# Kernel tuning notes

Measured on AMD Instinct MI355X. Metric: run time of the kernel, lower is better.

Reference implementation:

```python
import jax, jax.numpy as jnp
import numpy as np

CH = 512
RED = 16

def setup_inputs() -> dict:
    key = jax.random.key(0)
    ks = jax.random.split(key, 8)
    cq = CH // RED
    s = 0.02
    return {
        "x": jax.random.normal(ks[0], (4, CH, 64, 64), dtype=jnp.float32),
        "wq": jax.random.normal(ks[1], (cq, CH), dtype=jnp.float32) * s,
        "bq": jnp.zeros((cq,), dtype=jnp.float32),
        "wk": jax.random.normal(ks[2], (cq, CH), dtype=jnp.float32) * s,
        "bk": jnp.zeros((cq,), dtype=jnp.float32),
        "wv": jax.random.normal(ks[3], (CH, CH), dtype=jnp.float32) * s,
        "bv": jnp.zeros((CH,), dtype=jnp.float32),
        "gamma_pa": jnp.zeros((1,), dtype=jnp.float32),
        "gamma_ca": jnp.zeros((1,), dtype=jnp.float32),
    }

def _position_attention(x, wq, bq, wk, bk, wv, bv, gamma):
    B, C, H, W = x.shape
    xf = x.reshape(B, C, H * W)                     # [B, C, N]
    # 1x1 convs = per-pixel linear maps over channels
    q = jnp.einsum('oc,bcn->bon', wq, xf) + bq[None, :, None]   # [B, Cq, N]
    k = jnp.einsum('oc,bcn->bon', wk, xf) + bk[None, :, None]   # [B, Cq, N]
    v = jnp.einsum('oc,bcn->bon', wv, xf) + bv[None, :, None]   # [B, C,  N]
    # attention over key positions, no sqrt(d) scaling (faithful to DANet)
    energy = jnp.einsum('bcn,bcm->bnm', q, k)       # [B, N, N]
    attn = jax.nn.softmax(energy, axis=-1)
    out = jnp.einsum('bcm,bnm->bcn', v, attn)       # value @ attn^T
    out = out.reshape(B, C, H, W)
    return gamma * out + x

def _channel_attention(x, gamma):
    B, C, H, W = x.shape
    xf = x.reshape(B, C, H * W)                     # [B, C, N]
    energy = jnp.einsum('bcn,bdn->bcd', xf, xf)     # [B, C, C]
    energy_new = jnp.max(energy, axis=-1, keepdims=True) - energy
    attn = jax.nn.softmax(energy_new, axis=-1)
    out = jnp.einsum('bcd,bdn->bcn', attn, xf).reshape(B, C, H, W)
    return gamma * out + x

def reference(x, wq, bq, wk, bk, wv, bv, gamma_pa, gamma_ca):
    pa = _position_attention(x, wq, bq, wk, bk, wv, bv, gamma_pa)
    ca = _channel_attention(x, gamma_ca)
    return pa + ca
```

## Files before the change

### kernel.cpp

```cpp
#include <hip/hip_runtime.h>

#define CH   512
#define NPIX 4096
#define CQ   32
#define MR   640
#define NB   4

typedef unsigned short u16;
typedef __bf16 bf16x8 __attribute__((ext_vector_type(8)));
typedef float  f32x4  __attribute__((ext_vector_type(4)));
typedef unsigned int uint4v __attribute__((ext_vector_type(4)));
typedef unsigned int uint2v __attribute__((ext_vector_type(2)));

__device__ __forceinline__ u16 f2bf(float f) {
  union { float f; unsigned int u; } v; v.f = f;
  unsigned int r = v.u + 0x7FFFu + ((v.u >> 16) & 1u);
  return (u16)(r >> 16);
}

__device__ __forceinline__ void gload_lds16(const u16* g, u16* l) {
  __builtin_amdgcn_global_load_lds(
      (const __attribute__((address_space(1))) unsigned int*)g,
      (__attribute__((address_space(3))) unsigned int*)l, 16, 0, 0);
}

__device__ __forceinline__ int xcd_swz(int flat, int nwg) {
  if (nwg & 7) return flat;
  return (flat & 7) * (nwg >> 3) + (flat >> 3);
}

__global__ void k_prep_w(const float* __restrict__ wq, const float* __restrict__ bq,
                         const float* __restrict__ wk, const float* __restrict__ bk,
                         const float* __restrict__ wv, const float* __restrict__ bv,
                         u16* __restrict__ Wb, float* __restrict__ biasS) {
  int idx = blockIdx.x * 256 + threadIdx.x;
  if (idx < MR * CH) {
    int r = idx >> 9, c = idx & 511;
    float v = 0.f;
    if (r < 512)      v = wv[r * CH + c];
    else if (r < 544) v = wq[(r - 512) * CH + c];
    else if (r < 576) v = wk[(r - 544) * CH + c];
    Wb[idx] = f2bf(v);
  }
  if (idx < MR) {
    float v = 0.f;
    if (idx < 512)      v = bv[idx];
    else if (idx < 544) v = bq[idx - 512];
    else if (idx < 576) v = bk[idx - 544];
    biasS[idx] = v;
  }
}

__global__ __launch_bounds__(256) void k_convert(const float* __restrict__ x,
                                                 u16* __restrict__ Xb,
                                                 u16* __restrict__ Xt) {
  __shared__ float tile[64][65];
  const int b = blockIdx.z, ct = blockIdx.y, nt = blockIdx.x;
  const int t = threadIdx.x, tn = t & 63, tg = t >> 6;
  const size_t xbase = ((size_t)b * CH + ct * 64) * NPIX + nt * 64;
#pragma unroll
  for (int i = 0; i < 16; ++i) {
    int cl = tg * 16 + i;
    float v = x[xbase + (size_t)cl * NPIX + tn];
    Xb[xbase + (size_t)cl * NPIX + tn] = f2bf(v);
    tile[cl][tn] = v;
  }
  __syncthreads();
  const size_t tbase = ((size_t)b * NPIX + nt * 64) * CH + ct * 64;
#pragma unroll
  for (int i = 0; i < 16; ++i) {
    int nl = tg * 16 + i;
    Xt[tbase + (size_t)nl * CH + tn] = f2bf(tile[tn][nl]);
  }
}

enum { EP_QKV = 0, EP_PART = 1 };

template <int EP>
__global__ __launch_bounds__(256) void gemm_nt(
    const u16* __restrict__ Aall, const u16* __restrict__ Ball,
    long sA, long sB, int K, int ld, int zBase,
    void* pa0, void* pa1, void* pa2, const float* pg) {
  __shared__ u16 Alds[128 * 32];
  __shared__ u16 Blds[128 * 32];
  const int nbx = gridDim.x, nby = gridDim.y;
  const int nwg = nbx * nby * gridDim.z;
  int flat = blockIdx.x + nbx * (blockIdx.y + nby * blockIdx.z);
  flat = xcd_swz(flat, nwg);
  const int bx = flat % nbx, by = (flat / nbx) % nby, bz = flat / (nbx * nby);

  const int t = threadIdx.x, l = t & 63, w = t >> 6;
  const int wr = w >> 1, wc = w & 1;
  size_t aoff, boff;
  if constexpr (EP == EP_PART) {
    aoff = (size_t)(bz >> 2) * sA + (size_t)(bz & 3) * 1024;
    boff = (size_t)(bz >> 2) * sB + (size_t)(bz & 3) * 1024;
  } else {
    aoff = (size_t)bz * sA;
    boff = (size_t)bz * sB;
  }
  const u16* A = Aall + aoff;
  const u16* B = Ball + boff;
  const int rowBase = bx * 128, colBase = by * 128;

  f32x4 acc[4][4];
#pragma unroll
  for (int i = 0; i < 4; ++i)
#pragma unroll
    for (int j = 0; j < 4; ++j) acc[i][j] = f32x4{0.f, 0.f, 0.f, 0.f};

  const int rs0 = l >> 2, cs0 = (l & 3) * 8;

  for (int k0 = 0; k0 < K; k0 += 32) {
    __syncthreads();
#pragma unroll
    for (int i = 0; i < 2; ++i) {
      int chunk = w * 2 + i;
      int r = chunk * 16 + rs0;
      gload_lds16(A + (size_t)(rowBase + r) * ld + k0 + cs0, Alds + chunk * 512);
      gload_lds16(B + (size_t)(colBase + r) * ld + k0 + cs0, Blds + chunk * 512);
    }
    __syncthreads();
    bf16x8 af[4], bfr[4];
#pragma unroll
    for (int i = 0; i < 4; ++i) {
      af[i]  = *(const bf16x8*)(Alds + (wr * 64 + i * 16 + (l & 15)) * 32 + (l >> 4) * 8);
      bfr[i] = *(const bf16x8*)(Blds + (wc * 64 + i * 16 + (l & 15)) * 32 + (l >> 4) * 8);
    }
#pragma unroll
    for (int i = 0; i < 4; ++i)
#pragma unroll
      for (int j = 0; j < 4; ++j)
        acc[i][j] = __builtin_amdgcn_mfma_f32_16x16x32_bf16(af[i], bfr[j], acc[i][j], 0, 0, 0);
  }

  const int b = zBase + bz;
  if constexpr (EP == EP_QKV) {
    u16* Vb = (u16*)pa0; u16* Qt = (u16*)pa1; u16* Kt = (u16*)pa2;
#pragma unroll
    for (int i = 0; i < 4; ++i)
#pragma unroll
      for (int r = 0; r < 4; ++r) {
        int row = rowBase + wr * 64 + i * 16 + (l >> 4) * 4 + r;
        if (row >= 576) continue;
        float bias = pg[row];
#pragma unroll
        for (int j = 0; j < 4; ++j) {
          int col = colBase + wc * 64 + j * 16 + (l & 15);
          u16 h = f2bf(acc[i][j][r] + bias);
          if (row < 512)      Vb[((size_t)b * CH + row) * NPIX + col] = h;
          else if (row < 544) Qt[((size_t)b * NPIX + col) * CQ + (row - 512)] = h;
          else                Kt[((size_t)b * NPIX + col) * CQ + (row - 544)] = h;
        }
      }
  } else {
    float* C = (float*)pa0;
#pragma unroll
    for (int i = 0; i < 4; ++i)
#pragma unroll
      for (int j = 0; j < 4; ++j)
#pragma unroll
        for (int r = 0; r < 4; ++r) {
          int row = rowBase + wr * 64 + i * 16 + (l >> 4) * 4 + r;
          int col = colBase + wc * 64 + j * 16 + (l & 15);
          C[((size_t)bz * CH + row) * CH + col] = acc[i][j][r];
        }
  }
}

__global__ __launch_bounds__(256, 2) void k_pa_fused(
    const u16* __restrict__ Qt, const u16* __restrict__ Kt,
    const u16* __restrict__ Vb, const u16* __restrict__ Aca,
    const u16* __restrict__ Xt, const float* __restrict__ x,
    float* __restrict__ out, const float* __restrict__ gpa) {
  __shared__ u16 Plds[64 * 64];
  __shared__ u16 Vlds[2][4][64 * 64];
  int flat = xcd_swz(blockIdx.x, gridDim.x);
  const int chalf = flat & 1, nt = (flat >> 1) & 63, b = flat >> 7;
  const int n0 = nt * 64;
  const int l = threadIdx.x & 63, w = threadIdx.x >> 6;
  const int lo = l & 15, hi = l >> 4;
  const int c0w = chalf * 256 + w * 64;

  const u16* Qtb = Qt + (size_t)b * NPIX * CQ;
  const u16* Ktb = Kt + (size_t)b * NPIX * CQ;
  const u16* Vbb = Vb + (size_t)b * CH * NPIX;
  const f32x4 zero = {0.f, 0.f, 0.f, 0.f};

  bf16x8 bq[4];
#pragma unroll
  for (int nf = 0; nf < 4; ++nf)
    bq[nf] = *(const bf16x8*)(Qtb + (size_t)(n0 + nf * 16 + lo) * CQ + hi * 8);

  f32x4 acc[4][4];
#pragma unroll
  for (int i = 0; i < 4; ++i)
#pragma unroll
    for (int j = 0; j < 4; ++j) acc[i][j] = zero;
  float rs[4] = {0.f, 0.f, 0.f, 0.f};

  const int vcolsw = (((l & 7) ^ (l >> 3)) << 3);
  const u16* vsrc0 = Vbb + (size_t)(c0w + (l >> 3)) * NPIX + vcolsw;

#define LDK(m) (*(const bf16x8*)(Ktb + (size_t)((m) + w * 16 + lo) * CQ + hi * 8))
#define STAGE_V(mm, X)                                                         \
  {                                                                            \
    u16* vb_ = &Vlds[X][w][0];                                                 \
    const u16* g_ = vsrc0 + (mm);                                              \
    _Pragma("unroll")                                                          \
    for (int s_ = 0; s_ < 8; ++s_)                                             \
      gload_lds16(g_ + (size_t)s_ * 8 * NPIX, vb_ + s_ * 512);                 \
  }

  bf16x8 kc = LDK(0), kn;
  STAGE_V(0, 0);
  const int pslot = w * 2 + (hi >> 1);

  for (int ti = 0; ti < 64; ++ti) {
    const int X = ti & 1;
    const int mnext = ((ti + 1) & 63) * 64;
    f32x4 s[4];
#pragma unroll
    for (int nf = 0; nf < 4; ++nf)
      s[nf] = __builtin_amdgcn_mfma_f32_16x16x32_bf16(kc, bq[nf], zero, 0, 0, 0);
    kn = LDK(mnext);
    unsigned int uu[4][2];
#pragma unroll
    for (int nf = 0; nf < 4; ++nf) {
      float p0 = __expf(s[nf][0]), p1 = __expf(s[nf][1]);
      float p2 = __expf(s[nf][2]), p3 = __expf(s[nf][3]);
      rs[nf] += (p0 + p1) + (p2 + p3);
      asm("v_cvt_pk_bf16_f32 %0, %1, %2" : "=v"(uu[nf][0]) : "v"(p0), "v"(p1));
      asm("v_cvt_pk_bf16_f32 %0, %1, %2" : "=v"(uu[nf][1]) : "v"(p2), "v"(p3));
    }
    __builtin_amdgcn_s_barrier();
    __builtin_amdgcn_sched_barrier(0);
#pragma unroll
    for (int nf = 0; nf < 4; ++nf) {
      int n_ = nf * 16 + lo;
      char* dst_ = (char*)Plds + n_ * 128 + ((pslot ^ (n_ & 7)) << 4) + (hi & 1) * 8;
      *(uint2v*)dst_ = uint2v{uu[nf][0], uu[nf][1]};
    }
    asm volatile("s_waitcnt lgkmcnt(0)" ::: "memory");
    __builtin_amdgcn_sched_barrier(0);
    __builtin_amdgcn_s_barrier();
    __builtin_amdgcn_sched_barrier(0);
    STAGE_V(mnext, X ^ 1);
    asm volatile("s_waitcnt vmcnt(9)" ::: "memory");
    __builtin_amdgcn_sched_barrier(0);
    __builtin_amdgcn_s_setprio(1);
#pragma unroll
    for (int h = 0; h < 2; ++h) {
      bf16x8 va[4], bp[4];
#pragma unroll
      for (int i = 0; i < 4; ++i) {
        int vr = i * 16 + lo;
        va[i] = *(const bf16x8*)((const char*)(&Vlds[X][w][0]) + vr * 128 +
                                 ((h * 64 + hi * 16) ^ ((lo & 7) << 4)));
      }
#pragma unroll
      for (int j = 0; j < 4; ++j) {
        int nn = j * 16 + lo;
        bp[j] = *(const bf16x8*)((const char*)Plds + nn * 128 +
                                 (((h * 4 + hi) ^ (nn & 7)) << 4));
      }
#pragma unroll
      for (int i = 0; i < 4; ++i)
#pragma unroll
        for (int j = 0; j < 4; ++j)
          acc[i][j] = __builtin_amdgcn_mfma_f32_16x16x32_bf16(va[i], bp[j], acc[i][j], 0, 0, 0);
    }
    __builtin_amdgcn_s_setprio(0);
    kc = kn;
  }
#undef STAGE_V
#undef LDK

  __syncthreads();
#pragma unroll
  for (int nf = 0; nf < 4; ++nf) {
    rs[nf] += __shfl_xor(rs[nf], 16);
    rs[nf] += __shfl_xor(rs[nf], 32);
  }
  float* rbuf = (float*)Plds;
  if (l < 16) {
#pragma unroll
    for (int nf = 0; nf < 4; ++nf) rbuf[w * 64 + nf * 16 + l] = rs[nf];
  }
  __syncthreads();
  const float gv = gpa[0];
  float rinv[4];
#pragma unroll
  for (int j = 0; j < 4; ++j)
    rinv[j] = gv / (rbuf[j * 16 + lo] + rbuf[64 + j * 16 + lo] +
                    rbuf[128 + j * 16 + lo] + rbuf[192 + j * 16 + lo]);
#pragma unroll
  for (int i = 0; i < 4; ++i)
#pragma unroll
    for (int j = 0; j < 4; ++j) acc[i][j] *= rinv[j];
  __syncthreads();

  const u16* Acab = Aca + (size_t)b * CH * CH;
  const u16* Xtb = Xt + (size_t)b * NPIX * CH;
  const int ar = l >> 2;
  const int acs = (((l & 3) ^ (ar & 3)) << 3);
  u16* aldsw = &Vlds[0][w][0];
  u16* xlds = &Plds[0];

  for (int k0 = 0; k0 < CH; k0 += 32) {
    __syncthreads();
#pragma unroll
    for (int cch = 0; cch < 4; ++cch)
      gload_lds16(Acab + (size_t)(c0w + cch * 16 + ar) * CH + k0 + acs,
                  aldsw + cch * 512);
    gload_lds16(Xtb + (size_t)(n0 + w * 16 + ar) * CH + k0 + acs, xlds + w * 512);
    __syncthreads();
    bf16x8 af[4], bfx[4];
#pragma unroll
    for (int i = 0; i < 4; ++i) {
      int r = i * 16 + lo;
      af[i] = *(const bf16x8*)((const char*)aldsw + r * 64 + ((hi ^ (r & 3)) << 4));
    }
#pragma unroll
    for (int j = 0; j < 4; ++j) {
      int nn = j * 16 + lo;
      bfx[j] = *(const bf16x8*)((const char*)xlds + nn * 64 + ((hi ^ (nn & 3)) << 4));
    }
#pragma unroll
    for (int i = 0; i < 4; ++i)
#pragma unroll
      for (int j = 0; j < 4; ++j)
        acc[i][j] = __builtin_amdgcn_mfma_f32_16x16x32_bf16(af[i], bfx[j], acc[i][j], 0, 0, 0);
  }

  float* outb = out + (size_t)b * CH * NPIX;
  const float* xb = x + (size_t)b * CH * NPIX;
#pragma unroll
  for (int i = 0; i < 4; ++i)
#pragma unroll
    for (int j = 0; j < 4; ++j)
#pragma unroll
      for (int r = 0; r < 4; ++r) {
        int c = c0w + i * 16 + hi * 4 + r;
        int n = n0 + j * 16 + lo;
        size_t idx = (size_t)c * NPIX + n;
        outb[idx] = acc[i][j][r] + 2.0f * xb[idx];
      }
}

__global__ __launch_bounds__(256) void k_ca_softmax(const float* __restrict__ CAEp,
                                                    u16* __restrict__ Aca,
                                                    const float* __restrict__ gca) {
  const int l = threadIdx.x & 63, w = threadIdx.x >> 6;
  const int row = blockIdx.x * 4 + w;
  const int b = row >> 9, r = row & 511;
  float en0[8];
#pragma unroll
  for (int i = 0; i < 8; ++i) en0[i] = 0.f;
#pragma unroll
  for (int ks = 0; ks < 4; ++ks) {
    const float* e = CAEp + (((size_t)(b * 4 + ks) * CH + r) * CH);
    f32x4 a = *(const f32x4*)(e + l * 8);
    f32x4 c = *(const f32x4*)(e + l * 8 + 4);
#pragma unroll
    for (int i = 0; i < 4; ++i) { en0[i] += a[i]; en0[4 + i] += c[i]; }
  }
  float m1 = en0[0];
#pragma unroll
  for (int i = 1; i < 8; ++i) m1 = fmaxf(m1, en0[i]);
  for (int o = 1; o < 64; o <<= 1) m1 = fmaxf(m1, __shfl_xor(m1, o));
  float en[8];
#pragma unroll
  for (int i = 0; i < 8; ++i) en[i] = m1 - en0[i];
  float m2 = en[0];
#pragma unroll
  for (int i = 1; i < 8; ++i) m2 = fmaxf(m2, en[i]);
  for (int o = 1; o < 64; o <<= 1) m2 = fmaxf(m2, __shfl_xor(m2, o));
  float p[8], s = 0.f;
#pragma unroll
  for (int i = 0; i < 8; ++i) { p[i] = __expf(en[i] - m2); s += p[i]; }
  for (int o = 1; o < 64; o <<= 1) s += __shfl_xor(s, o);
  const float inv = gca[0] / s;
  union { u16 h[8]; uint4v v; } u;
#pragma unroll
  for (int i = 0; i < 8; ++i) u.h[i] = f2bf(p[i] * inv);
  *(uint4v*)(Aca + (size_t)row * CH + l * 8) = u.v;
}

extern "C" void kernel_launch(void* const* d_in, const int* in_sizes, int n_in,
                              void* d_out, int out_size, void* d_ws, size_t ws_size,
                              hipStream_t stream) {
  const float* x   = (const float*)d_in[0];
  const float* wq  = (const float*)d_in[1];
  const float* bq  = (const float*)d_in[2];
  const float* wk  = (const float*)d_in[3];
  const float* bk  = (const float*)d_in[4];
  const float* wv  = (const float*)d_in[5];
  const float* bv  = (const float*)d_in[6];
  const float* gpa = (const float*)d_in[7];
  const float* gca = (const float*)d_in[8];
  float* out = (float*)d_out;

  char* wsp = (char*)d_ws;
  size_t off = 0;
  auto alloc = [&](size_t bytes) -> void* {
    void* p = (void*)(wsp + off);
    off = (off + bytes + 255) & ~(size_t)255;
    return p;
  };
  const size_t EB = (size_t)NB * CH * NPIX;
  u16*   Xb    = (u16*)alloc(EB * 2);
  u16*   Xt    = (u16*)alloc(EB * 2);
  u16*   Wb    = (u16*)alloc((size_t)MR * CH * 2);
  float* biasS = (float*)alloc((size_t)MR * 4);
  u16*   Vb    = (u16*)alloc(EB * 2);
  u16*   Qt    = (u16*)alloc((size_t)NB * NPIX * CQ * 2);
  u16*   Kt    = (u16*)alloc((size_t)NB * NPIX * CQ * 2);
  float* CAEp  = (float*)alloc((size_t)NB * 4 * CH * CH * 4);
  u16*   Aca   = (u16*)alloc((size_t)NB * CH * CH * 2);

  k_prep_w<<<(MR * CH + 255) / 256, 256, 0, stream>>>(wq, bq, wk, bk, wv, bv, Wb, biasS);
  k_convert<<<dim3(64, 8, NB), 256, 0, stream>>>(x, Xb, Xt);

  gemm_nt<EP_QKV><<<dim3(MR / 128, NPIX / 128, NB), 256, 0, stream>>>(
      Wb, Xt, 0L, (long)NPIX * CH, CH, CH, 0, Vb, Qt, Kt, biasS);

  gemm_nt<EP_PART><<<dim3(CH / 128, CH / 128, NB * 4), 256, 0, stream>>>(
      Xb, Xb, (long)CH * NPIX, (long)CH * NPIX, 1024, NPIX, 0,
      CAEp, nullptr, nullptr, nullptr);
  k_ca_softmax<<<NB * CH / 4, 256, 0, stream>>>(CAEp, Aca, gca);

  k_pa_fused<<<NB * (NPIX / 64) * 2, 256, 0, stream>>>(
      Qt, Kt, Vb, Aca, Xt, x, out, gpa);
}
```

Baseline: 183.0 us.

## Restructure fused PA kernel: 2-wave blocks, register-staged V, exp2 with prescaled Q

Recasts the fused position-attention kernel to 128-thread blocks that each cover 128 channels, doubling the grid. V tiles are no longer staged through LDS and are loaded directly into registers with double buffering. Each wave now computes 32 key rows of the energy tile, and the P tile in LDS is double-buffered, which removes one barrier per step. Q is prescaled by log2(e) in the QKV epilogue so the softmax can use the hardware exp2 instruction. The channel-attention GEMM tail also switches from LDS staging to register-prefetched global loads. The trade is more global/L2 traffic (each V and K row is fetched by more blocks) and higher register pressure in exchange for fewer barriers and less LDS use.

Result: slower. 248.1 us (+35.6%).

```diff
diff --git a/kernel.cpp b/kernel.cpp
--- a/kernel.cpp
+++ b/kernel.cpp
@@ -5,6 +5,7 @@
 #define CQ   32
 #define MR   640
 #define NB   4
+#define LOG2E 1.44269504088896340736f
 
 typedef unsigned short u16;
 typedef __bf16 bf16x8 __attribute__((ext_vector_type(8)));
@@ -16,6 +17,10 @@
   union { float f; unsigned int u; } v; v.f = f;
   unsigned int r = v.u + 0x7FFFu + ((v.u >> 16) & 1u);
   return (u16)(r >> 16);
+}
+
+__device__ __forceinline__ float exp2fast(float f) {
+  return __builtin_amdgcn_exp2f(f);
 }
 
 __device__ __forceinline__ void gload_lds16(const u16* g, u16* l) {
@@ -144,10 +149,11 @@
         int row = rowBase + wr * 64 + i * 16 + (l >> 4) * 4 + r;
         if (row >= 576) continue;
         float bias = pg[row];
+        float scale = (row >= 512 && row < 544) ? LOG2E : 1.0f;
 #pragma unroll
         for (int j = 0; j < 4; ++j) {
           int col = colBase + wc * 64 + j * 16 + (l & 15);
-          u16 h = f2bf(acc[i][j][r] + bias);
+          u16 h = f2bf((acc[i][j][r] + bias) * scale);
           if (row < 512)      Vb[((size_t)b * CH + row) * NPIX + col] = h;
           else if (row < 544) Qt[((size_t)b * NPIX + col) * CQ + (row - 512)] = h;
           else                Kt[((size_t)b * NPIX + col) * CQ + (row - 544)] = h;
@@ -168,19 +174,19 @@
   }
 }
 
-__global__ __launch_bounds__(256, 2) void k_pa_fused(
+__global__ __launch_bounds__(128, 2) void k_pa_fused(
     const u16* __restrict__ Qt, const u16* __restrict__ Kt,
     const u16* __restrict__ Vb, const u16* __restrict__ Aca,
     const u16* __restrict__ Xt, const float* __restrict__ x,
     float* __restrict__ out, const float* __restrict__ gpa) {
-  __shared__ u16 Plds[64 * 64];
-  __shared__ u16 Vlds[2][4][64 * 64];
+  __shared__ u16 Plds[2][64 * 64];
+
   int flat = xcd_swz(blockIdx.x, gridDim.x);
-  const int chalf = flat & 1, nt = (flat >> 1) & 63, b = flat >> 7;
+  const int nt = flat & 63, cq = (flat >> 6) & 3, b = flat >> 8;
   const int n0 = nt * 64;
   const int l = threadIdx.x & 63, w = threadIdx.x >> 6;
   const int lo = l & 15, hi = l >> 4;
-  const int c0w = chalf * 256 + w * 64;
+  const int c0w = cq * 128 + w * 64;
 
   const u16* Qtb = Qt + (size_t)b * NPIX * CQ;
   const u16* Ktb = Kt + (size_t)b * NPIX * CQ;
@@ -199,82 +205,79 @@
     for (int j = 0; j < 4; ++j) acc[i][j] = zero;
   float rs[4] = {0.f, 0.f, 0.f, 0.f};
 
-  const int vcolsw = (((l & 7) ^ (l >> 3)) << 3);
-  const u16* vsrc0 = Vbb + (size_t)(c0w + (l >> 3)) * NPIX + vcolsw;
-
-#define LDK(m) (*(const bf16x8*)(Ktb + (size_t)((m) + w * 16 + lo) * CQ + hi * 8))
-#define STAGE_V(mm, X)                                                         \
+#define LDK(m, ml) (*(const bf16x8*)(Ktb + (size_t)((m) + w * 32 + (ml) * 16 + lo) * CQ + hi * 8))
+#define LDV(m, i, h) (*(const bf16x8*)(Vbb + (size_t)(c0w + (i) * 16 + lo) * NPIX + (m) + (h) * 32 + hi * 8))
+
+#define PA_STEP(Kc0, Kc1, Kn0, Kn1, Vc, Vn, X, mnext)                          \
   {                                                                            \
-    u16* vb_ = &Vlds[X][w][0];                                                 \
-    const u16* g_ = vsrc0 + (mm);                                              \
+    f32x4 s_[4][2];                                                            \
     _Pragma("unroll")                                                          \
-    for (int s_ = 0; s_ < 8; ++s_)                                             \
-      gload_lds16(g_ + (size_t)s_ * 8 * NPIX, vb_ + s_ * 512);                 \
-  }
-
-  bf16x8 kc = LDK(0), kn;
-  STAGE_V(0, 0);
-  const int pslot = w * 2 + (hi >> 1);
-
-  for (int ti = 0; ti < 64; ++ti) {
-    const int X = ti & 1;
-    const int mnext = ((ti + 1) & 63) * 64;
-    f32x4 s[4];
-#pragma unroll
-    for (int nf = 0; nf < 4; ++nf)
-      s[nf] = __builtin_amdgcn_mfma_f32_16x16x32_bf16(kc, bq[nf], zero, 0, 0, 0);
-    kn = LDK(mnext);
-    unsigned int uu[4][2];
-#pragma unroll
-    for (int nf = 0; nf < 4; ++nf) {
-      float p0 = __expf(s[nf][0]), p1 = __expf(s[nf][1]);
-      float p2 = __expf(s[nf][2]), p3 = __expf(s[nf][3]);
-      rs[nf] += (p0 + p1) + (p2 + p3);
-      asm("v_cvt_pk_bf16_f32 %0, %1, %2" : "=v"(uu[nf][0]) : "v"(p0), "v"(p1));
-      asm("v_cvt_pk_bf16_f32 %0, %1, %2" : "=v"(uu[nf][1]) : "v"(p2), "v"(p3));
-    }
-    __builtin_amdgcn_s_barrier();
-    __builtin_amdgcn_sched_barrier(0);
-#pragma unroll
-    for (int nf = 0; nf < 4; ++nf) {
-      int n_ = nf * 16 + lo;
-      char* dst_ = (char*)Plds + n_ * 128 + ((pslot ^ (n_ & 7)) << 4) + (hi & 1) * 8;
-      *(uint2v*)dst_ = uint2v{uu[nf][0], uu[nf][1]};
-    }
-    asm volatile("s_waitcnt lgkmcnt(0)" ::: "memory");
-    __builtin_amdgcn_sched_barrier(0);
-    __builtin_amdgcn_s_barrier();
-    __builtin_amdgcn_sched_barrier(0);
-    STAGE_V(mnext, X ^ 1);
-    asm volatile("s_waitcnt vmcnt(9)" ::: "memory");
-    __builtin_amdgcn_sched_barrier(0);
-    __builtin_amdgcn_s_setprio(1);
-#pragma unroll
-    for (int h = 0; h < 2; ++h) {
-      bf16x8 va[4], bp[4];
-#pragma unroll
-      for (int i = 0; i < 4; ++i) {
-        int vr = i * 16 + lo;
-        va[i] = *(const bf16x8*)((const char*)(&Vlds[X][w][0]) + vr * 128 +
-                                 ((h * 64 + hi * 16) ^ ((lo & 7) << 4)));
-      }
-#pragma unroll
-      for (int j = 0; j < 4; ++j) {
-        int nn = j * 16 + lo;
-        bp[j] = *(const bf16x8*)((const char*)Plds + nn * 128 +
-                                 (((h * 4 + hi) ^ (nn & 7)) << 4));
-      }
-#pragma unroll
-      for (int i = 0; i < 4; ++i)
-#pragma unroll
-        for (int j = 0; j < 4; ++j)
-          acc[i][j] = __builtin_amdgcn_mfma_f32_16x16x32_bf16(va[i], bp[j], acc[i][j], 0, 0, 0);
-    }
-    __builtin_amdgcn_s_setprio(0);
-    kc = kn;
-  }
-#undef STAGE_V
+    for (int nf_ = 0; nf_ < 4; ++nf_) {                                        \
+      s_[nf_][0] = __builtin_amdgcn_mfma_f32_16x16x32_bf16(Kc0, bq[nf_], zero, 0, 0, 0); \
+      s_[nf_][1] = __builtin_amdgcn_mfma_f32_16x16x32_bf16(Kc1, bq[nf_], zero, 0, 0, 0); \
+    }                                                                          \
+    Kn0 = LDK(mnext, 0);                                                       \
+    Kn1 = LDK(mnext, 1);                                                       \
+    _Pragma("unroll")                                                          \
+    for (int nf_ = 0; nf_ < 4; ++nf_) {                                        \
+      int n_ = nf_ * 16 + lo;                                                  \
+      char* rowp_ = (char*)(Plds[X]) + n_ * 128 + (hi & 1) * 8;                \
+      _Pragma("unroll")                                                        \
+      for (int ml_ = 0; ml_ < 2; ++ml_) {                                      \
+        float p0_ = exp2fast(s_[nf_][ml_][0]), p1_ = exp2fast(s_[nf_][ml_][1]);\
+        float p2_ = exp2fast(s_[nf_][ml_][2]), p3_ = exp2fast(s_[nf_][ml_][3]);\
+        rs[nf_] += (p0_ + p1_) + (p2_ + p3_);                                  \
+        unsigned int u0_, u1_;                                                 \
+        asm("v_cvt_pk_bf16_f32 %0, %1, %2" : "=v"(u0_) : "v"(p0_), "v"(p1_));  \
+        asm("v_cvt_pk_bf16_f32 %0, %1, %2" : "=v"(u1_) : "v"(p2_), "v"(p3_));  \
+        int slot_ = w * 4 + ml_ * 2 + (hi >> 1);                               \
+        *(uint2v*)(rowp_ + ((slot_ ^ (n_ & 7)) << 4)) = uint2v{u0_, u1_};      \
+      }                                                                        \
+    }                                                                          \
+    asm volatile("s_waitcnt lgkmcnt(0)" ::: "memory");                         \
+    __builtin_amdgcn_sched_barrier(0);                                         \
+    __builtin_amdgcn_s_barrier();                                              \
+    __builtin_amdgcn_sched_barrier(0);                                         \
+    _Pragma("unroll")                                                          \
+    for (int i_ = 0; i_ < 4; ++i_) {                                           \
+      Vn[i_ * 2 + 0] = LDV(mnext, i_, 0);                                      \
+      Vn[i_ * 2 + 1] = LDV(mnext, i_, 1);                                      \
+    }                                                                          \
+    __builtin_amdgcn_s_setprio(1);                                             \
+    _Pragma("unroll")                                                          \
+    for (int h_ = 0; h_ < 2; ++h_) {                                           \
+      bf16x8 bp_[4];                                                           \
+      _Pragma("unroll")                                                        \
+      for (int j_ = 0; j_ < 4; ++j_) {                                         \
+        int nn_ = j_ * 16 + lo;                                                \
+        bp_[j_] = *(const bf16x8*)((const char*)(Plds[X]) + nn_ * 128 +        \
+                                   (((h_ * 4 + hi) ^ (nn_ & 7)) << 4));        \
+      }                                                                        \
+      _Pragma("unroll")                                                        \
+      for (int i_ = 0; i_ < 4; ++i_)                                           \
+        _Pragma("unroll")                                                      \
+        for (int j_ = 0; j_ < 4; ++j_)                                         \
+          acc[i_][j_] = __builtin_amdgcn_mfma_f32_16x16x32_bf16(               \
+              Vc[i_ * 2 + h_], bp_[j_], acc[i_][j_], 0, 0, 0);                 \
+    }                                                                          \
+    __builtin_amdgcn_s_setprio(0);                                             \
+  }
+
+  bf16x8 kA0 = LDK(0, 0), kA1 = LDK(0, 1), kB0, kB1;
+  bf16x8 vA[8], vB[8];
+#pragma unroll
+  for (int i = 0; i < 4; ++i) {
+    vA[i * 2 + 0] = LDV(0, i, 0);
+    vA[i * 2 + 1] = LDV(0, i, 1);
+  }
+
+  for (int ti = 0; ti < 64; ti += 2) {
+    PA_STEP(kA0, kA1, kB0, kB1, vA, vB, 0, (((ti + 1) & 63) * 64));
+    PA_STEP(kB0, kB1, kA0, kA1, vB, vA, 1, (((ti + 2) & 63) * 64));
+  }
+#undef PA_STEP
 #undef LDK
+#undef LDV
 
   __syncthreads();
 #pragma unroll
@@ -292,46 +295,38 @@
   float rinv[4];
 #pragma unroll
   for (int j = 0; j < 4; ++j)
-    rinv[j] = gv / (rbuf[j * 16 + lo] + rbuf[64 + j * 16 + lo] +
-                    rbuf[128 + j * 16 + lo] + rbuf[192 + j * 16 + lo]);
+    rinv[j] = gv / (rbuf[j * 16 + lo] + rbuf[64 + j * 16 + lo]);
 #pragma unroll
   for (int i = 0; i < 4; ++i)
 #pragma unroll
     for (int j = 0; j < 4; ++j) acc[i][j] *= rinv[j];
-  __syncthreads();
 
   const u16* Acab = Aca + (size_t)b * CH * CH;
   const u16* Xtb = Xt + (size_t)b * NPIX * CH;
-  const int ar = l >> 2;
-  const int acs = (((l & 3) ^ (ar & 3)) << 3);
-  u16* aldsw = &Vlds[0][w][0];
-  u16* xlds = &Plds[0];
-
-  for (int k0 = 0; k0 < CH; k0 += 32) {
-    __syncthreads();
-#pragma unroll
-    for (int cch = 0; cch < 4; ++cch)
-      gload_lds16(Acab + (size_t)(c0w + cch * 16 + ar) * CH + k0 + acs,
-                  aldsw + cch * 512);
-    gload_lds16(Xtb + (size_t)(n0 + w * 16 + ar) * CH + k0 + acs, xlds + w * 512);
-    __syncthreads();
-    bf16x8 af[4], bfx[4];
-#pragma unroll
-    for (int i = 0; i < 4; ++i) {
-      int r = i * 16 + lo;
-      af[i] = *(const bf16x8*)((const char*)aldsw + r * 64 + ((hi ^ (r & 3)) << 4));
-    }
-#pragma unroll
-    for (int j = 0; j < 4; ++j) {
-      int nn = j * 16 + lo;
-      bfx[j] = *(const bf16x8*)((const char*)xlds + nn * 64 + ((hi ^ (nn & 3)) << 4));
-    }
-#pragma unroll
-    for (int i = 0; i < 4; ++i)
-#pragma unroll
-      for (int j = 0; j < 4; ++j)
-        acc[i][j] = __builtin_amdgcn_mfma_f32_16x16x32_bf16(af[i], bfx[j], acc[i][j], 0, 0, 0);
-  }
+#define LDA_CA(k0, i) (*(const bf16x8*)(Acab + (size_t)(c0w + (i) * 16 + lo) * CH + (k0) + hi * 8))
+#define LDX_CA(k0, j) (*(const bf16x8*)(Xtb + (size_t)(n0 + (j) * 16 + lo) * CH + (k0) + hi * 8))
+#define CA_MFMA(AF, BX)                                                        \
+  _Pragma("unroll")                                                            \
+  for (int i_ = 0; i_ < 4; ++i_)                                               \
+    _Pragma("unroll")                                                          \
+    for (int j_ = 0; j_ < 4; ++j_)                                             \
+      acc[i_][j_] = __builtin_amdgcn_mfma_f32_16x16x32_bf16(AF[i_], BX[j_], acc[i_][j_], 0, 0, 0);
+
+  bf16x8 caA[4], cxA[4], caB[4], cxB[4];
+#pragma unroll
+  for (int i = 0; i < 4; ++i) { caA[i] = LDA_CA(0, i); cxA[i] = LDX_CA(0, i); }
+  for (int k0 = 0; k0 < CH; k0 += 64) {
+#pragma unroll
+    for (int i = 0; i < 4; ++i) { caB[i] = LDA_CA(k0 + 32, i); cxB[i] = LDX_CA(k0 + 32, i); }
+    CA_MFMA(caA, cxA);
+    int k2 = (k0 + 64) & (CH - 1);
+#pragma unroll
+    for (int i = 0; i < 4; ++i) { caA[i] = LDA_CA(k2, i); cxA[i] = LDX_CA(k2, i); }
+    CA_MFMA(caB, cxB);
+  }
+#undef LDA_CA
+#undef LDX_CA
+#undef CA_MFMA
 
   float* outb = out + (size_t)b * CH * NPIX;
   const float* xb = x + (size_t)b * CH * NPIX;
@@ -430,6 +425,6 @@
       CAEp, nullptr, nullptr, nullptr);
   k_ca_softmax<<<NB * CH / 4, 256, 0, stream>>>(CAEp, Aca, gca);
 
-  k_pa_fused<<<NB * (NPIX / 64) * 2, 256, 0, stream>>>(
+  k_pa_fused<<<NB * 4 * (NPIX / 64), 128, 0, stream>>>(
       Qt, Kt, Vb, Aca, Xt, x, out, gpa);
 }
```
